# Kernel optimization log

Measured on AMD Instinct MI355X. Metric: run time of the kernel, lower is better.

## Reference

```python
import jax, jax.numpy as jnp
import numpy as np

B, S, HID = 1, 2048, 4096
NH, NKV, HD = 32, 8, 128
INIT, RECENT, HEAVY = 128, 512, 512
THETA = 10000.0


def _rope(x, pos):
    # x: [B,H,S,D]; standard Llama rotary embedding (rotate_half convention)
    d = x.shape[-1]
    inv = 1.0 / (THETA ** (jnp.arange(0, d, 2, dtype=jnp.float32) / d))
    ang = pos[:, None] * inv[None, :]                      # [S, D/2]
    cos = jnp.concatenate([jnp.cos(ang), jnp.cos(ang)], -1)  # [S, D]
    sin = jnp.concatenate([jnp.sin(ang), jnp.sin(ang)], -1)
    x1, x2 = x[..., : d // 2], x[..., d // 2:]
    rot = jnp.concatenate([-x2, x1], -1)
    return x * cos + rot * sin


def setup_inputs() -> dict:
    key = jax.random.key(0)
    ks = jax.random.split(key, 5)
    s = 1.0 / np.sqrt(HID)
    return {
        "hidden_states": jax.random.normal(ks[0], (B, S, HID), jnp.float32),
        "wq": jax.random.normal(ks[1], (HID, NH * HD), jnp.float32) * s,
        "wk": jax.random.normal(ks[2], (HID, NKV * HD), jnp.float32) * s,
        "wv": jax.random.normal(ks[3], (HID, NKV * HD), jnp.float32) * s,
        "wo": jax.random.normal(ks[4], (NH * HD, HID), jnp.float32) * s,
    }


def reference(hidden_states, wq, wk, wv, wo):
    # QKV projections (no bias, per attention_bias=False)
    q = (hidden_states @ wq).reshape(B, S, NH, HD).transpose(0, 2, 1, 3)   # [B,NH,S,D]
    k = (hidden_states @ wk).reshape(B, S, NKV, HD).transpose(0, 2, 1, 3)  # [B,NKV,S,D]
    v = (hidden_states @ wv).reshape(B, S, NKV, HD).transpose(0, 2, 1, 3)
    pos = jnp.arange(S, dtype=jnp.float32)
    q = _rope(q, pos)
    k = _rope(k, pos)
    # repeat_kv for GQA
    rep = NH // NKV
    k = jnp.repeat(k, rep, axis=1)
    v = jnp.repeat(v, rep, axis=1)

    scores = jnp.einsum('bhqd,bhkd->bhqk', q, k) / np.sqrt(HD)  # [B,NH,S,S]

    qi = jnp.arange(S)[:, None]
    ki = jnp.arange(S)[None, :]
    causal = ki <= qi
    # causal_heavy_recent_mask: tril(diag = k - q - recent) with [:, :init] = False
    middle = (ki <= qi - RECENT) & (ki >= INIT)   # heavy-hitter eligible region
    base = causal & jnp.logical_not(middle)       # init + recent tokens always kept

    neg = jnp.finfo(scores.dtype).min
    mid_scores = jnp.where(middle[None, None], scores, neg)
    _, idx = jax.lax.top_k(mid_scores, HEAVY)     # [B,NH,S,HEAVY]
    flat = idx.reshape(-1, HEAVY)
    rows = jnp.arange(flat.shape[0])[:, None]
    heavy = jnp.zeros((flat.shape[0], S), dtype=bool).at[rows, flat].set(True)
    heavy = heavy.reshape(B, NH, S, S) & middle[None, None]

    mask = base[None, None] | heavy
    attn = jax.nn.softmax(jnp.where(mask, scores, neg), axis=-1)
    out = jnp.einsum('bhqk,bhkd->bhqd', attn, v)
    out = out.transpose(0, 2, 1, 3).reshape(B, S, NH * HD)
    return out @ wo
```

## Files before the change

kernel.cpp:

```cpp
#include <hip/hip_runtime.h>
#include <math.h>

#define S_LEN 2048
#define HID_N 4096
#define NH 32
#define NKV 8
#define HD 128
#define INIT_N 128
#define RECENT_N 512
#define HEAVY_N 512
#define SCALE_QK 0.08838834764831845f

typedef __attribute__((ext_vector_type(8))) short short8;
typedef __attribute__((ext_vector_type(4))) float float4v;

__device__ __forceinline__ unsigned short f2bf(float f) {
  unsigned u = __float_as_uint(f);
  unsigned r = (u + 0x7FFFu + ((u >> 16) & 1u)) >> 16;
  return (unsigned short)r;
}

__device__ __forceinline__ float bf2f(unsigned u) { return __uint_as_float(u << 16); }

__device__ __forceinline__ unsigned fkey16(unsigned u) {
  return (u & 0x8000u) ? ((~u) & 0xFFFFu) : (u | 0x8000u);
}

__device__ __forceinline__ void gld_lds16(const unsigned short* g, unsigned short* l) {
  __builtin_amdgcn_global_load_lds(
      (const __attribute__((address_space(1))) unsigned int*)g,
      (__attribute__((address_space(3))) unsigned int*)l, 16, 0, 0);
}

__global__ __launch_bounds__(256) void cast_bf16x8(const float* __restrict__ x,
                                                   unsigned short* __restrict__ y, int n) {
  int i = (blockIdx.x * 256 + threadIdx.x) << 3;
  if (i >= n) return;
  float4 a = *(const float4*)(x + i);
  float4 b = *(const float4*)(x + i + 4);
  union { unsigned short u[8]; short8 v; } o;
  o.u[0] = f2bf(a.x); o.u[1] = f2bf(a.y); o.u[2] = f2bf(a.z); o.u[3] = f2bf(a.w);
  o.u[4] = f2bf(b.x); o.u[5] = f2bf(b.y); o.u[6] = f2bf(b.z); o.u[7] = f2bf(b.w);
  *(short8*)(y + i) = o.v;
}

__global__ __launch_bounds__(256) void transpose_cast(const float* __restrict__ w,
                                                      unsigned short* __restrict__ wt,
                                                      int R, int C, int ldw) {
  __shared__ unsigned short t[64][65];
  const int c0 = blockIdx.x * 64;
  const int r0 = blockIdx.y * 64;
  const int tx = threadIdx.x & 63;
  const int ty = threadIdx.x >> 6;
#pragma unroll
  for (int i = 0; i < 16; ++i)
    t[ty + 4 * i][tx] = f2bf(w[(size_t)(r0 + ty + 4 * i) * ldw + c0 + tx]);
  __syncthreads();
#pragma unroll
  for (int i = 0; i < 16; ++i)
    wt[(size_t)(c0 + ty + 4 * i) * R + r0 + tx] = t[tx][ty + 4 * i];
}

__global__ __launch_bounds__(256) void gemm_bf16(const unsigned short* __restrict__ A,
                                                 const unsigned short* __restrict__ BT,
                                                 float* __restrict__ C,
                                                 int M, int N, int K) {
  __shared__ __align__(16) unsigned short As[128 * 32];
  __shared__ __align__(16) unsigned short Bs[128 * 32];
  const int tid = threadIdx.x;
  const int lane = tid & 63;
  const int wid = tid >> 6;
  const int m0 = blockIdx.y * 128;
  const int n0 = blockIdx.x * 128;
  const int wm = (wid & 1) * 64;
  const int wn = (wid >> 1) * 64;
  const int col = lane & 15;
  const int quad = lane >> 4;

  float4v acc[4][4] = {};

  const int crow = tid >> 2;
  const int ckc = (tid & 3) << 3;

  for (int k0 = 0; k0 < K; k0 += 32) {
#pragma unroll
    for (int i = 0; i < 2; ++i) {
      const int row = i * 64 + crow;
      unsigned short* la = &As[(i * 256 + wid * 64) << 3];
      unsigned short* lb = &Bs[(i * 256 + wid * 64) << 3];
      gld_lds16(A + (size_t)(m0 + row) * K + k0 + ckc, la);
      gld_lds16(BT + (size_t)(n0 + row) * K + k0 + ckc, lb);
    }
    __syncthreads();

    short8 af[4], bf[4];
#pragma unroll
    for (int i = 0; i < 4; ++i) {
      af[i] = *(const short8*)&As[((wm + 16 * i + col) << 5) + (quad << 3)];
      bf[i] = *(const short8*)&Bs[((wn + 16 * i + col) << 5) + (quad << 3)];
    }
#pragma unroll
    for (int i = 0; i < 4; ++i)
#pragma unroll
      for (int j = 0; j < 4; ++j)
        acc[i][j] = __builtin_amdgcn_mfma_f32_16x16x32_bf16(af[i], bf[j], acc[i][j], 0, 0, 0);
    __syncthreads();
  }

#pragma unroll
  for (int i = 0; i < 4; ++i)
#pragma unroll
    for (int j = 0; j < 4; ++j) {
      size_t base = (size_t)(m0 + wm + 16 * i + quad * 4) * N + n0 + wn + 16 * j + col;
      C[base] = acc[i][j][0];
      C[base + N] = acc[i][j][1];
      C[base + 2 * (size_t)N] = acc[i][j][2];
      C[base + 3 * (size_t)N] = acc[i][j][3];
    }
}

__global__ __launch_bounds__(256) void rope_cast(const float* __restrict__ x,
                                                 unsigned short* __restrict__ y,
                                                 int nheads, int ldx, int ldy) {
  int idx = blockIdx.x * 256 + threadIdx.x;
  int i = idx & 63;
  int rest = idx >> 6;
  int hh = rest % nheads;
  int s = rest / nheads;
  if (s >= S_LEN) return;
  const float* p = x + (size_t)s * ldx + hh * HD;
  unsigned short* o = y + (size_t)s * ldy + hh * HD;
  float inv = (float)(1.0 / pow(10000.0, (double)(2 * i) / 128.0));
  float ang = (float)s * inv;
  float c = cosf(ang);
  float sn = sinf(ang);
  float x1 = p[i];
  float x2 = p[i + 64];
  o[i] = f2bf(x1 * c - x2 * sn);
  o[i + 64] = f2bf(x2 * c + x1 * sn);
}

template <int SMAX>
__global__ __launch_bounds__(512, 4)
void attn_mfma(const unsigned short* __restrict__ qb,
               const unsigned short* __restrict__ kb,
               const unsigned short* __restrict__ vt,
               unsigned short* __restrict__ ao16, int qbase) {
  const int qi0 = (qbase + blockIdx.x) << 4;
  const int h = blockIdx.y;
  const int g = h >> 2;
  const int tid = threadIdx.x;
  const int lane = tid & 63;
  const int wid = tid >> 6;
  const int col = lane & 15;
  const int quad = lane >> 4;
  const int nkm = qi0 + 16;
  const int nkm32 = (nkm + 31) & ~31;

  __shared__ __align__(16) unsigned short sc[16 * SMAX];
  __shared__ float sumv[16];

  short8 qf[4];
  {
    const unsigned short* qrow = qb + (size_t)(qi0 + col) * (NH * HD) + h * HD + (quad << 3);
#pragma unroll
    for (int dt = 0; dt < 4; ++dt) qf[dt] = *(const short8*)(qrow + dt * 32);
  }
  const int ntiles = nkm >> 4;
  int t = wid;
  for (; t + 8 < ntiles; t += 16) {
    const int k0a = t << 4;
    const int k0b = (t + 8) << 4;
    const unsigned short* kra = kb + (size_t)(k0a + col) * (NKV * HD) + g * HD + (quad << 3);
    const unsigned short* krb = kb + (size_t)(k0b + col) * (NKV * HD) + g * HD + (quad << 3);
    short8 kfa[4], kfb[4];
#pragma unroll
    for (int dt = 0; dt < 4; ++dt) kfa[dt] = *(const short8*)(kra + dt * 32);
#pragma unroll
    for (int dt = 0; dt < 4; ++dt) kfb[dt] = *(const short8*)(krb + dt * 32);
    float4v acca = {}, accb = {};
#pragma unroll
    for (int dt = 0; dt < 4; ++dt) {
      acca = __builtin_amdgcn_mfma_f32_16x16x32_bf16(qf[dt], kfa[dt], acca, 0, 0, 0);
      accb = __builtin_amdgcn_mfma_f32_16x16x32_bf16(qf[dt], kfb[dt], accb, 0, 0, 0);
    }
#pragma unroll
    for (int r = 0; r < 4; ++r) {
      int q = (quad << 2) + r;
      sc[(q * SMAX + k0a + col) ^ ((q & 7) << 3)] = f2bf(acca[r] * SCALE_QK);
      sc[(q * SMAX + k0b + col) ^ ((q & 7) << 3)] = f2bf(accb[r] * SCALE_QK);
    }
  }
  if (t < ntiles) {
    const int k0 = t << 4;
    const unsigned short* krow = kb + (size_t)(k0 + col) * (NKV * HD) + g * HD + (quad << 3);
    float4v acc = {};
#pragma unroll
    for (int dt = 0; dt < 4; ++dt) {
      short8 kf = *(const short8*)(krow + dt * 32);
      acc = __builtin_amdgcn_mfma_f32_16x16x32_bf16(qf[dt], kf, acc, 0, 0, 0);
    }
#pragma unroll
    for (int r = 0; r < 4; ++r) {
      int q = (quad << 2) + r;
      sc[(q * SMAX + k0 + col) ^ ((q & 7) << 3)] = f2bf(acc[r] * SCALE_QK);
    }
  }
  __syncthreads();

  const unsigned long long lmlt = (1ull << lane) - 1ull;
#pragma unroll 1
  for (int rr = 0; rr < 2; ++rr) {
    const int r = (wid << 1) + rr;
    const int qi = qi0 + r;
    const int mhi = qi - RECENT_N;
    const int m = mhi - INIT_N + 1;
    const bool need = (SMAX > 1024) && (m > HEAVY_N);
    const unsigned swz = (r & 7) << 3;
    const int rbase = r * SMAX;

    unsigned T = 0, rem = 0;
    if (need) {
      unsigned myk[22];
#pragma unroll
      for (int j = 0; j < 11; ++j) {
        int off = (lane + (j << 6)) << 1;
        unsigned u = *(const unsigned*)&sc[(rbase + INIT_N + off) ^ swz];
        unsigned f0 = fkey16(u & 0xFFFFu);
        unsigned f1 = fkey16(u >> 16);
        myk[2 * j] = (off < m) ? f0 : 0u;
        myk[2 * j + 1] = (off + 1 < m) ? f1 : 0u;
      }
      unsigned prefix = 0, rm = HEAVY_N;
#pragma unroll 1
      for (int bit = 15; bit >= 0; --bit) {
        unsigned target = (prefix >> bit) | 1u;
        unsigned cnt = 0;
#pragma unroll
        for (int j = 0; j < 22; ++j)
          cnt += (unsigned)__popcll(__ballot((myk[j] >> bit) == target));
        if (cnt >= rm) prefix |= (1u << bit);
        else rm -= cnt;
      }
      T = prefix;
      rem = rm;
    }

    float mx = -3.402823466e38f;
#pragma unroll 1
    for (int c0 = 0; c0 <= qi; c0 += 128) {
      int k2 = c0 + (lane << 1);
      unsigned u = *(const unsigned*)&sc[(rbase + k2) ^ swz];
      float s0 = bf2f(u & 0xFFFFu);
      float s1 = bf2f(u >> 16);
      if (k2 <= qi) mx = fmaxf(mx, s0);
      if (k2 + 1 <= qi) mx = fmaxf(mx, s1);
    }
#pragma unroll
    for (int off = 32; off; off >>= 1) mx = fmaxf(mx, __shfl_xor(mx, off, 64));

    float sum = 0.f;
    unsigned cum = 0;
#pragma unroll 1
    for (int c0 = 0; c0 < nkm32; c0 += 128) {
      int k2 = c0 + (lane << 1);
      int idx = (rbase + k2) ^ swz;
      unsigned u = *(const unsigned*)&sc[idx];
      bool ic0 = k2 <= qi, ic1 = (k2 + 1) <= qi;
      bool sel0, sel1;
      if (!need) {
        sel0 = ic0;
        sel1 = ic1;
      } else {
        bool mid0 = ic0 && (k2 >= INIT_N) && (k2 <= mhi);
        bool mid1 = ic1 && (k2 + 1 >= INIT_N) && (k2 + 1 <= mhi);
        unsigned f0 = fkey16(u & 0xFFFFu);
        unsigned f1 = fkey16(u >> 16);
        unsigned long long eq0 = __ballot(mid0 && (f0 == T));
        unsigned long long eq1 = __ballot(mid1 && (f1 == T));
        unsigned pre0 = cum + (unsigned)__popcll(eq0 & lmlt) + (unsigned)__popcll(eq1 & lmlt);
        unsigned pre1 = pre0 + (unsigned)((eq0 >> lane) & 1ull);
        sel0 = ic0 && (!mid0 || (f0 > T) || ((f0 == T) && (pre0 < rem)));
        sel1 = ic1 && (!mid1 || (f1 > T) || ((f1 == T) && (pre1 < rem)));
        cum += (unsigned)__popcll(eq0) + (unsigned)__popcll(eq1);
      }
      float e0 = sel0 ? __expf(bf2f(u & 0xFFFFu) - mx) : 0.f;
      float e1 = sel1 ? __expf(bf2f(u >> 16) - mx) : 0.f;
      sum += e0 + e1;
      *(unsigned*)&sc[idx] = (unsigned)f2bf(e0) | ((unsigned)f2bf(e1) << 16);
    }
#pragma unroll
    for (int off = 32; off; off >>= 1) sum += __shfl_xor(sum, off, 64);
    if (lane == 0) sumv[r] = sum;
  }
  __syncthreads();

  float4v a0 = {}, b0 = {};
  const int db = wid << 4;
  const unsigned short* vrow = vt + (size_t)(g * HD + db + col) * S_LEN + (quad << 3);
  const unsigned pswz = (unsigned)((col & 7) << 3);
  int k0 = 0;
  for (; k0 + 32 < nkm32; k0 += 64) {
    short8 pf0 = *(const short8*)&sc[(col * SMAX + k0 + (quad << 3)) ^ pswz];
    short8 pf1 = *(const short8*)&sc[(col * SMAX + k0 + 32 + (quad << 3)) ^ pswz];
    short8 v0 = *(const short8*)(vrow + k0);
    short8 v1 = *(const short8*)(vrow + k0 + 32);
    a0 = __builtin_amdgcn_mfma_f32_16x16x32_bf16(pf0, v0, a0, 0, 0, 0);
    b0 = __builtin_amdgcn_mfma_f32_16x16x32_bf16(pf1, v1, b0, 0, 0, 0);
  }
  if (k0 < nkm32) {
    short8 pf = *(const short8*)&sc[(col * SMAX + k0 + (quad << 3)) ^ pswz];
    short8 v0 = *(const short8*)(vrow + k0);
    a0 = __builtin_amdgcn_mfma_f32_16x16x32_bf16(pf, v0, a0, 0, 0, 0);
  }
  a0 += b0;
#pragma unroll
  for (int r = 0; r < 4; ++r) {
    int qq = (quad << 2) + r;
    float inv = 1.0f / sumv[qq];
    size_t o = (size_t)(qi0 + qq) * (NH * HD) + h * HD + db;
    ao16[o + col] = f2bf(a0[r] * inv);
  }
}

extern "C" void kernel_launch(void* const* d_in, const int* in_sizes, int n_in,
                              void* d_out, int out_size, void* d_ws, size_t ws_size,
                              hipStream_t stream) {
  const float* hidden = (const float*)d_in[0];
  const float* wq = (const float*)d_in[1];
  const float* wk = (const float*)d_in[2];
  const float* wv = (const float*)d_in[3];
  const float* wo = (const float*)d_in[4];
  float* out = (float*)d_out;

  float* ws = (float*)d_ws;
  const size_t M1 = 1024 * 1024;
  float* qkv = ws;
  unsigned short* qb16 = (unsigned short*)(ws + 12 * M1);
  unsigned short* hb = (unsigned short*)(ws + 16 * M1);
  unsigned short* aob = hb;
  unsigned short* wqkvT = (unsigned short*)(ws + 20 * M1);
  unsigned short* woT = wqkvT;
  unsigned short* kb16 = (unsigned short*)(ws + 28 * M1);
  unsigned short* vT16 = (unsigned short*)(ws + 29 * M1);

  dim3 blk(256);
  const int NE = S_LEN * HID_N;

  cast_bf16x8<<<NE / 2048, blk, 0, stream>>>(hidden, hb, NE);
  transpose_cast<<<dim3(HID_N / 64, HID_N / 64), blk, 0, stream>>>(wq, wqkvT, HID_N, HID_N, HID_N);
  transpose_cast<<<dim3((NKV * HD) / 64, HID_N / 64), blk, 0, stream>>>(
      wk, wqkvT + (size_t)HID_N * HID_N, HID_N, NKV * HD, NKV * HD);
  transpose_cast<<<dim3((NKV * HD) / 64, HID_N / 64), blk, 0, stream>>>(
      wv, wqkvT + (size_t)(HID_N + NKV * HD) * HID_N, HID_N, NKV * HD, NKV * HD);

  gemm_bf16<<<dim3(6144 / 128, S_LEN / 128), blk, 0, stream>>>(hb, wqkvT, qkv, S_LEN, 6144, HID_N);

  transpose_cast<<<dim3(HID_N / 64, HID_N / 64), blk, 0, stream>>>(wo, woT, NH * HD, HID_N, HID_N);

  rope_cast<<<(S_LEN * NH * 64) / 256, blk, 0, stream>>>(qkv, qb16, NH, 6144, NH * HD);
  rope_cast<<<(S_LEN * NKV * 64) / 256, blk, 0, stream>>>(qkv + HID_N, kb16, NKV, 6144, NKV * HD);
  transpose_cast<<<dim3((NKV * HD) / 64, S_LEN / 64), blk, 0, stream>>>(
      qkv + HID_N + NKV * HD, vT16, S_LEN, NKV * HD, 6144);

  attn_mfma<2048><<<dim3(64, NH), dim3(512), 0, stream>>>(qb16, kb16, vT16, aob, 64);
  attn_mfma<1024><<<dim3(64, NH), dim3(512), 0, stream>>>(qb16, kb16, vT16, aob, 0);

  gemm_bf16<<<dim3(HID_N / 128, S_LEN / 128), blk, 0, stream>>>(aob, woT, out, S_LEN, HID_N, NH * HD);
}
```

Baseline: 850.9 us.

## Double attention block to 1024 threads, one row per wave, split PV over keys

Attention blocks now run 16 waves instead of 8. Each wave handles one query row in the top-k selection and softmax phase. The PV product is split across two wave groups over key halves, and partial results are reduced through a new shared-memory buffer. Query tiles are also interleaved so small and large causal tiles alternate across blocks for load balance. The QK phase drops its two-tile unroll. The aim is more parallelism in the serial per-row selection, paid for with an extra barrier, more LDS, and register pressure from 1024-thread launch bounds.

```diff
diff --git a/kernel.cpp b/kernel.cpp
--- a/kernel.cpp
+++ b/kernel.cpp
@@ -141,12 +141,14 @@
 }
 
 template <int SMAX>
-__global__ __launch_bounds__(512, 4)
+__global__ __launch_bounds__(1024, 8)
 void attn_mfma(const unsigned short* __restrict__ qb,
                const unsigned short* __restrict__ kb,
                const unsigned short* __restrict__ vt,
                unsigned short* __restrict__ ao16, int qbase) {
-  const int qi0 = (qbase + blockIdx.x) << 4;
+  const int bx = blockIdx.x;
+  const int tile = (bx & 1) ? (63 - (bx >> 1)) : (bx >> 1);
+  const int qi0 = (qbase + tile) << 4;
   const int h = blockIdx.y;
   const int g = h >> 2;
   const int tid = threadIdx.x;
@@ -158,6 +160,7 @@
   const int nkm32 = (nkm + 31) & ~31;
 
   __shared__ __align__(16) unsigned short sc[16 * SMAX];
+  __shared__ float po[16][132];
   __shared__ float sumv[16];
 
   short8 qf[4];
@@ -167,31 +170,7 @@
     for (int dt = 0; dt < 4; ++dt) qf[dt] = *(const short8*)(qrow + dt * 32);
   }
   const int ntiles = nkm >> 4;
-  int t = wid;
-  for (; t + 8 < ntiles; t += 16) {
-    const int k0a = t << 4;
-    const int k0b = (t + 8) << 4;
-    const unsigned short* kra = kb + (size_t)(k0a + col) * (NKV * HD) + g * HD + (quad << 3);
-    const unsigned short* krb = kb + (size_t)(k0b + col) * (NKV * HD) + g * HD + (quad << 3);
-    short8 kfa[4], kfb[4];
-#pragma unroll
-    for (int dt = 0; dt < 4; ++dt) kfa[dt] = *(const short8*)(kra + dt * 32);
-#pragma unroll
-    for (int dt = 0; dt < 4; ++dt) kfb[dt] = *(const short8*)(krb + dt * 32);
-    float4v acca = {}, accb = {};
-#pragma unroll
-    for (int dt = 0; dt < 4; ++dt) {
-      acca = __builtin_amdgcn_mfma_f32_16x16x32_bf16(qf[dt], kfa[dt], acca, 0, 0, 0);
-      accb = __builtin_amdgcn_mfma_f32_16x16x32_bf16(qf[dt], kfb[dt], accb, 0, 0, 0);
-    }
-#pragma unroll
-    for (int r = 0; r < 4; ++r) {
-      int q = (quad << 2) + r;
-      sc[(q * SMAX + k0a + col) ^ ((q & 7) << 3)] = f2bf(acca[r] * SCALE_QK);
-      sc[(q * SMAX + k0b + col) ^ ((q & 7) << 3)] = f2bf(accb[r] * SCALE_QK);
-    }
-  }
-  if (t < ntiles) {
+  for (int t = wid; t < ntiles; t += 16) {
     const int k0 = t << 4;
     const unsigned short* krow = kb + (size_t)(k0 + col) * (NKV * HD) + g * HD + (quad << 3);
     float4v acc = {};
@@ -209,9 +188,8 @@
   __syncthreads();
 
   const unsigned long long lmlt = (1ull << lane) - 1ull;
-#pragma unroll 1
-  for (int rr = 0; rr < 2; ++rr) {
-    const int r = (wid << 1) + rr;
+  {
+    const int r = wid;
     const int qi = qi0 + r;
     const int mhi = qi - RECENT_N;
     const int m = mhi - INIT_N + 1;
@@ -295,12 +273,17 @@
   }
   __syncthreads();
 
+  const int kmid = ((nkm32 >> 1) + 31) & ~31;
+  const bool hi = wid >= 8;
+  const int w8 = wid & 7;
+  const int db = w8 << 4;
+  const int kstart = hi ? kmid : 0;
+  const int kend = hi ? nkm32 : kmid;
   float4v a0 = {}, b0 = {};
-  const int db = wid << 4;
   const unsigned short* vrow = vt + (size_t)(g * HD + db + col) * S_LEN + (quad << 3);
   const unsigned pswz = (unsigned)((col & 7) << 3);
-  int k0 = 0;
-  for (; k0 + 32 < nkm32; k0 += 64) {
+  int k0 = kstart;
+  for (; k0 + 32 < kend; k0 += 64) {
     short8 pf0 = *(const short8*)&sc[(col * SMAX + k0 + (quad << 3)) ^ pswz];
     short8 pf1 = *(const short8*)&sc[(col * SMAX + k0 + 32 + (quad << 3)) ^ pswz];
     short8 v0 = *(const short8*)(vrow + k0);
@@ -308,18 +291,26 @@
     a0 = __builtin_amdgcn_mfma_f32_16x16x32_bf16(pf0, v0, a0, 0, 0, 0);
     b0 = __builtin_amdgcn_mfma_f32_16x16x32_bf16(pf1, v1, b0, 0, 0, 0);
   }
-  if (k0 < nkm32) {
+  if (k0 < kend) {
     short8 pf = *(const short8*)&sc[(col * SMAX + k0 + (quad << 3)) ^ pswz];
     short8 v0 = *(const short8*)(vrow + k0);
     a0 = __builtin_amdgcn_mfma_f32_16x16x32_bf16(pf, v0, a0, 0, 0, 0);
   }
   a0 += b0;
-#pragma unroll
-  for (int r = 0; r < 4; ++r) {
-    int qq = (quad << 2) + r;
-    float inv = 1.0f / sumv[qq];
-    size_t o = (size_t)(qi0 + qq) * (NH * HD) + h * HD + db;
-    ao16[o + col] = f2bf(a0[r] * inv);
+  if (hi) {
+#pragma unroll
+    for (int r = 0; r < 4; ++r) po[(quad << 2) + r][db + col] = a0[r];
+  }
+  __syncthreads();
+  if (!hi) {
+#pragma unroll
+    for (int r = 0; r < 4; ++r) {
+      int qq = (quad << 2) + r;
+      float inv = 1.0f / sumv[qq];
+      float val = a0[r] + po[qq][db + col];
+      size_t o = (size_t)(qi0 + qq) * (NH * HD) + h * HD + db;
+      ao16[o + col] = f2bf(val * inv);
+    }
   }
 }
 
@@ -363,8 +354,8 @@
   transpose_cast<<<dim3((NKV * HD) / 64, S_LEN / 64), blk, 0, stream>>>(
       qkv + HID_N + NKV * HD, vT16, S_LEN, NKV * HD, 6144);
 
-  attn_mfma<2048><<<dim3(64, NH), dim3(512), 0, stream>>>(qb16, kb16, vT16, aob, 64);
-  attn_mfma<1024><<<dim3(64, NH), dim3(512), 0, stream>>>(qb16, kb16, vT16, aob, 0);
+  attn_mfma<2048><<<dim3(64, NH), dim3(1024), 0, stream>>>(qb16, kb16, vT16, aob, 64);
+  attn_mfma<1024><<<dim3(64, NH), dim3(1024), 0, stream>>>(qb16, kb16, vT16, aob, 0);
 
   gemm_bf16<<<dim3(HID_N / 128, S_LEN / 128), blk, 0, stream>>>(aob, woT, out, S_LEN, HID_N, NH * HD);
 }
```

After: 880.7 us. +3.5%, slower.

## Replace bf16 GEMM with 256x256-tile double-buffered pipelined MFMA kernel

Applied to the files above, without the earlier changes.

Replaces the simple 128x128 single-buffered GEMM with a 256x256-tile kernel using 8 waves. It double-buffers K-chunks of 64 in 128KB of LDS, interleaves async global-to-LDS loads with MFMA phases under explicit vmcnt waits and barriers, and raises MFMA priority with setprio. It also remaps workgroup IDs to group tiles for cache locality. The goal is to hide global load latency and raise data reuse per tile in both projection GEMMs. The cost is fewer workgroups (192 and 128), which may underfill the 256 CUs, and fragile hand-tuned wait counts.

```diff
diff --git a/kernel.cpp b/kernel.cpp
--- a/kernel.cpp
+++ b/kernel.cpp
@@ -31,6 +31,8 @@
       (const __attribute__((address_space(1))) unsigned int*)g,
       (__attribute__((address_space(3))) unsigned int*)l, 16, 0, 0);
 }
+
+#define VMCNT(n) asm volatile("s_waitcnt vmcnt(" #n ")" ::: "memory")
 
 __global__ __launch_bounds__(256) void cast_bf16x8(const float* __restrict__ x,
                                                    unsigned short* __restrict__ y, int n) {
@@ -61,62 +63,169 @@
     wt[(size_t)(c0 + ty + 4 * i) * R + r0 + tx] = t[tx][ty + 4 * i];
 }
 
-__global__ __launch_bounds__(256) void gemm_bf16(const unsigned short* __restrict__ A,
-                                                 const unsigned short* __restrict__ BT,
-                                                 float* __restrict__ C,
-                                                 int M, int N, int K) {
-  __shared__ __align__(16) unsigned short As[128 * 32];
-  __shared__ __align__(16) unsigned short Bs[128 * 32];
+__global__ __launch_bounds__(512, 2)
+void gemm256(const unsigned short* __restrict__ A,
+             const unsigned short* __restrict__ BT,
+             float* __restrict__ C, int M, int N, int K) {
+  __shared__ __align__(16) unsigned short lds[65536];
   const int tid = threadIdx.x;
   const int lane = tid & 63;
   const int wid = tid >> 6;
-  const int m0 = blockIdx.y * 128;
-  const int n0 = blockIdx.x * 128;
-  const int wm = (wid & 1) * 64;
-  const int wn = (wid >> 1) * 64;
+  const int wr = wid >> 2;
+  const int wc = wid & 3;
   const int col = lane & 15;
   const int quad = lane >> 4;
 
-  float4v acc[4][4] = {};
-
-  const int crow = tid >> 2;
-  const int ckc = (tid & 3) << 3;
-
-  for (int k0 = 0; k0 < K; k0 += 32) {
-#pragma unroll
-    for (int i = 0; i < 2; ++i) {
-      const int row = i * 64 + crow;
-      unsigned short* la = &As[(i * 256 + wid * 64) << 3];
-      unsigned short* lb = &Bs[(i * 256 + wid * 64) << 3];
-      gld_lds16(A + (size_t)(m0 + row) * K + k0 + ckc, la);
-      gld_lds16(BT + (size_t)(n0 + row) * K + k0 + ckc, lb);
-    }
-    __syncthreads();
-
-    short8 af[4], bf[4];
-#pragma unroll
-    for (int i = 0; i < 4; ++i) {
-      af[i] = *(const short8*)&As[((wm + 16 * i + col) << 5) + (quad << 3)];
-      bf[i] = *(const short8*)&Bs[((wn + 16 * i + col) << 5) + (quad << 3)];
-    }
-#pragma unroll
-    for (int i = 0; i < 4; ++i)
-#pragma unroll
-      for (int j = 0; j < 4; ++j)
-        acc[i][j] = __builtin_amdgcn_mfma_f32_16x16x32_bf16(af[i], bf[j], acc[i][j], 0, 0, 0);
-    __syncthreads();
-  }
-
-#pragma unroll
-  for (int i = 0; i < 4; ++i)
-#pragma unroll
-    for (int j = 0; j < 4; ++j) {
-      size_t base = (size_t)(m0 + wm + 16 * i + quad * 4) * N + n0 + wn + 16 * j + col;
-      C[base] = acc[i][j][0];
-      C[base + N] = acc[i][j][1];
-      C[base + 2 * (size_t)N] = acc[i][j][2];
-      C[base + 3 * (size_t)N] = acc[i][j][3];
-    }
+  const int gx = gridDim.x;
+  const int nwg = gx * gridDim.y;
+  int lin = blockIdx.y * gx + blockIdx.x;
+  lin = (lin & 7) * (nwg >> 3) + (lin >> 3);
+  const int m0 = (lin / gx) << 8;
+  const int n0 = (lin % gx) << 8;
+  const int NT = K >> 6;
+
+  const int sdst = wid << 9;
+  const int grow = tid >> 3;
+  const int gcol = (tid & 7) << 3;
+
+#define STG2(G, B0_, LOFF, RB0, RB1, KC)                                      \
+  do {                                                                        \
+    gld_lds16(G + (size_t)((B0_) + (RB0) + grow) * K + (KC) + gcol,           \
+              &lds[(LOFF) + (RB0) * 64 + sdst]);                              \
+    gld_lds16(G + (size_t)((B0_) + (RB1) + grow) * K + (KC) + gcol,           \
+              &lds[(LOFF) + (RB1) * 64 + sdst]);                              \
+  } while (0)
+
+  float4v acc[8][4] = {};
+
+  STG2(BT, n0, 32768, 0, 64, 0);
+  STG2(BT, n0, 32768, 128, 192, 0);
+  STG2(A, m0, 0, 0, 128, 0);
+  STG2(A, m0, 0, 64, 192, 0);
+  if (NT > 1) {
+    STG2(BT, n0, 32768 + 16384, 0, 64, 64);
+    STG2(BT, n0, 32768 + 16384, 128, 192, 64);
+    STG2(A, m0, 16384, 0, 128, 64);
+    VMCNT(8);
+  } else {
+    VMCNT(2);
+  }
+  __builtin_amdgcn_s_barrier();
+
+#pragma unroll 1
+  for (int t = 0; t < NT; ++t) {
+    const int cb = (t & 1) << 14;
+    const int nb = cb ^ 16384;
+    const int cbB = 32768 + cb;
+    const int kc1 = (t + 1) << 6;
+    const int kc2 = (t + 2) << 6;
+    const bool h1 = (t + 1) < NT;
+    const bool h2 = (t + 2) < NT;
+    const int abase = cb + (wr * 128 + col) * 64 + (quad << 3);
+
+    short8 b8[4][2];
+#pragma unroll
+    for (int ni = 0; ni < 4; ++ni)
+#pragma unroll
+      for (int kk = 0; kk < 2; ++kk)
+        b8[ni][kk] = *(const short8*)&lds[cbB + (wc * 64 + ni * 16 + col) * 64 +
+                                          (quad << 3) + kk * 32];
+    {
+      short8 x0 = *(const short8*)&lds[abase + 0 * 64];
+      short8 x1 = *(const short8*)&lds[abase + 0 * 64 + 32];
+      short8 x2 = *(const short8*)&lds[abase + 16 * 64];
+      short8 x3 = *(const short8*)&lds[abase + 16 * 64 + 32];
+      if (h1) STG2(A, m0, nb, 64, 192, kc1);
+      __builtin_amdgcn_s_barrier();
+      asm volatile("s_waitcnt lgkmcnt(0)" ::: "memory");
+      __builtin_amdgcn_sched_barrier(0);
+      __builtin_amdgcn_s_setprio(1);
+#pragma unroll
+      for (int ni = 0; ni < 4; ++ni) {
+        acc[0][ni] = __builtin_amdgcn_mfma_f32_16x16x32_bf16(x0, b8[ni][0], acc[0][ni], 0, 0, 0);
+        acc[0][ni] = __builtin_amdgcn_mfma_f32_16x16x32_bf16(x1, b8[ni][1], acc[0][ni], 0, 0, 0);
+        acc[1][ni] = __builtin_amdgcn_mfma_f32_16x16x32_bf16(x2, b8[ni][0], acc[1][ni], 0, 0, 0);
+        acc[1][ni] = __builtin_amdgcn_mfma_f32_16x16x32_bf16(x3, b8[ni][1], acc[1][ni], 0, 0, 0);
+      }
+      __builtin_amdgcn_s_setprio(0);
+      __builtin_amdgcn_s_barrier();
+    }
+    {
+      short8 x0 = *(const short8*)&lds[abase + 32 * 64];
+      short8 x1 = *(const short8*)&lds[abase + 32 * 64 + 32];
+      short8 x2 = *(const short8*)&lds[abase + 48 * 64];
+      short8 x3 = *(const short8*)&lds[abase + 48 * 64 + 32];
+      if (h2) STG2(BT, n0, cbB, 0, 64, kc2);
+      if (h2) { VMCNT(10); } else if (h1) { VMCNT(8); } else { VMCNT(0); }
+      __builtin_amdgcn_s_barrier();
+      asm volatile("s_waitcnt lgkmcnt(0)" ::: "memory");
+      __builtin_amdgcn_sched_barrier(0);
+      __builtin_amdgcn_s_setprio(1);
+#pragma unroll
+      for (int ni = 0; ni < 4; ++ni) {
+        acc[2][ni] = __builtin_amdgcn_mfma_f32_16x16x32_bf16(x0, b8[ni][0], acc[2][ni], 0, 0, 0);
+        acc[2][ni] = __builtin_amdgcn_mfma_f32_16x16x32_bf16(x1, b8[ni][1], acc[2][ni], 0, 0, 0);
+        acc[3][ni] = __builtin_amdgcn_mfma_f32_16x16x32_bf16(x2, b8[ni][0], acc[3][ni], 0, 0, 0);
+        acc[3][ni] = __builtin_amdgcn_mfma_f32_16x16x32_bf16(x3, b8[ni][1], acc[3][ni], 0, 0, 0);
+      }
+      __builtin_amdgcn_s_setprio(0);
+      __builtin_amdgcn_s_barrier();
+    }
+    {
+      short8 x0 = *(const short8*)&lds[abase + 64 * 64];
+      short8 x1 = *(const short8*)&lds[abase + 64 * 64 + 32];
+      short8 x2 = *(const short8*)&lds[abase + 80 * 64];
+      short8 x3 = *(const short8*)&lds[abase + 80 * 64 + 32];
+      if (h2) STG2(BT, n0, cbB, 128, 192, kc2);
+      __builtin_amdgcn_s_barrier();
+      asm volatile("s_waitcnt lgkmcnt(0)" ::: "memory");
+      __builtin_amdgcn_sched_barrier(0);
+      __builtin_amdgcn_s_setprio(1);
+#pragma unroll
+      for (int ni = 0; ni < 4; ++ni) {
+        acc[4][ni] = __builtin_amdgcn_mfma_f32_16x16x32_bf16(x0, b8[ni][0], acc[4][ni], 0, 0, 0);
+        acc[4][ni] = __builtin_amdgcn_mfma_f32_16x16x32_bf16(x1, b8[ni][1], acc[4][ni], 0, 0, 0);
+        acc[5][ni] = __builtin_amdgcn_mfma_f32_16x16x32_bf16(x2, b8[ni][0], acc[5][ni], 0, 0, 0);
+        acc[5][ni] = __builtin_amdgcn_mfma_f32_16x16x32_bf16(x3, b8[ni][1], acc[5][ni], 0, 0, 0);
+      }
+      __builtin_amdgcn_s_setprio(0);
+      __builtin_amdgcn_s_barrier();
+    }
+    {
+      short8 x0 = *(const short8*)&lds[abase + 96 * 64];
+      short8 x1 = *(const short8*)&lds[abase + 96 * 64 + 32];
+      short8 x2 = *(const short8*)&lds[abase + 112 * 64];
+      short8 x3 = *(const short8*)&lds[abase + 112 * 64 + 32];
+      if (h2) STG2(A, m0, cb, 0, 128, kc2);
+      if (h2) { VMCNT(8); } else if (h1) { VMCNT(2); }
+      __builtin_amdgcn_s_barrier();
+      asm volatile("s_waitcnt lgkmcnt(0)" ::: "memory");
+      __builtin_amdgcn_sched_barrier(0);
+      __builtin_amdgcn_s_setprio(1);
+#pragma unroll
+      for (int ni = 0; ni < 4; ++ni) {
+        acc[6][ni] = __builtin_amdgcn_mfma_f32_16x16x32_bf16(x0, b8[ni][0], acc[6][ni], 0, 0, 0);
+        acc[6][ni] = __builtin_amdgcn_mfma_f32_16x16x32_bf16(x1, b8[ni][1], acc[6][ni], 0, 0, 0);
+        acc[7][ni] = __builtin_amdgcn_mfma_f32_16x16x32_bf16(x2, b8[ni][0], acc[7][ni], 0, 0, 0);
+        acc[7][ni] = __builtin_amdgcn_mfma_f32_16x16x32_bf16(x3, b8[ni][1], acc[7][ni], 0, 0, 0);
+      }
+      __builtin_amdgcn_s_setprio(0);
+      __builtin_amdgcn_s_barrier();
+    }
+  }
+
+#pragma unroll
+  for (int mi = 0; mi < 8; ++mi)
+#pragma unroll
+    for (int ni = 0; ni < 4; ++ni) {
+      size_t base = (size_t)(m0 + wr * 128 + mi * 16 + (quad << 2)) * N +
+                    n0 + wc * 64 + ni * 16 + col;
+      C[base] = acc[mi][ni][0];
+      C[base + N] = acc[mi][ni][1];
+      C[base + 2 * (size_t)N] = acc[mi][ni][2];
+      C[base + 3 * (size_t)N] = acc[mi][ni][3];
+    }
+#undef STG2
 }
 
 __global__ __launch_bounds__(256) void rope_cast(const float* __restrict__ x,
@@ -354,7 +463,7 @@
   transpose_cast<<<dim3((NKV * HD) / 64, HID_N / 64), blk, 0, stream>>>(
       wv, wqkvT + (size_t)(HID_N + NKV * HD) * HID_N, HID_N, NKV * HD, NKV * HD);
 
-  gemm_bf16<<<dim3(6144 / 128, S_LEN / 128), blk, 0, stream>>>(hb, wqkvT, qkv, S_LEN, 6144, HID_N);
+  gemm256<<<dim3(6144 / 256, S_LEN / 256), dim3(512), 0, stream>>>(hb, wqkvT, qkv, S_LEN, 6144, HID_N);
 
   transpose_cast<<<dim3(HID_N / 64, HID_N / 64), blk, 0, stream>>>(wo, woT, NH * HD, HID_N, HID_N);
 
@@ -366,5 +475,5 @@
   attn_mfma<2048><<<dim3(64, NH), dim3(512), 0, stream>>>(qb16, kb16, vT16, aob, 64);
   attn_mfma<1024><<<dim3(64, NH), dim3(512), 0, stream>>>(qb16, kb16, vT16, aob, 0);
 
-  gemm_bf16<<<dim3(HID_N / 128, S_LEN / 128), blk, 0, stream>>>(aob, woT, out, S_LEN, HID_N, NH * HD);
-}
+  gemm256<<<dim3(HID_N / 256, S_LEN / 256), dim3(512), 0, stream>>>(aob, woT, out, S_LEN, HID_N, NH * HD);
+}
```

Result: slower. 909.2 us (+6.8%).
